# Optimization experiments

Hardware: AMD Instinct MI355X
Metric: run time of the kernel (lower is better)

The kernel has to match this reference:

```python
import jax, jax.numpy as jnp
import numpy as np
import math

B, S, N, F = 512, 72, 5, 10
H, C = 4, 32          # GAT heads, per-head dim
D = H * C             # 128 d_model
L, FF = 3, 256        # transformer layers, ffn dim
K, NS = 6, 5          # horizons, stations
EPS = 1e-5


def layer_norm(x, g, b):
    m = x.mean(-1, keepdims=True)
    v = ((x - m) ** 2).mean(-1, keepdims=True)
    return (x - m) / jnp.sqrt(v + EPS) * g + b


def setup_inputs() -> dict:
    key = jax.random.key(0)
    ks = jax.random.split(key, 16)
    # all 20 directed non-self edges of the 5-node graph
    src, dst = np.nonzero(1 - np.eye(N, dtype=np.int32))
    edge_index = jnp.asarray(np.stack([src, dst]).astype(np.int32))
    w = lambda k, shp: (jax.random.normal(k, shp, jnp.float32) * 0.05)
    return {
        "x": jax.random.normal(ks[0], (B, S, N, F), jnp.float32),
        "edge_index": edge_index,
        "gat_w": w(ks[1], (F, D)),
        "gat_att_src": w(ks[2], (H, C)),
        "gat_att_dst": w(ks[3], (H, C)),
        "gat_bias": jnp.zeros((D,), jnp.float32),
        "gat_ln_g": jnp.ones((D,), jnp.float32),
        "gat_ln_b": jnp.zeros((D,), jnp.float32),
        "qkv_w": w(ks[4], (L, 3 * D, D)),
        "qkv_b": jnp.zeros((L, 3 * D), jnp.float32),
        "out_w": w(ks[5], (L, D, D)),
        "out_b": jnp.zeros((L, D), jnp.float32),
        "ln1_g": jnp.ones((L, D), jnp.float32),
        "ln1_b": jnp.zeros((L, D), jnp.float32),
        "ff1_w": w(ks[6], (L, FF, D)),
        "ff1_b": jnp.zeros((L, FF), jnp.float32),
        "ff2_w": w(ks[7], (L, D, FF)),
        "ff2_b": jnp.zeros((L, D), jnp.float32),
        "ln2_g": jnp.ones((L, D), jnp.float32),
        "ln2_b": jnp.zeros((L, D), jnp.float32),
        "h1_w": w(ks[8], (K, D // 2, D)),
        "h1_b": jnp.zeros((K, D // 2), jnp.float32),
        "h2_w": w(ks[9], (K, NS, D // 2)),
        "h2_b": jnp.zeros((K, NS), jnp.float32),
    }


def reference(x, edge_index, gat_w, gat_att_src, gat_att_dst, gat_bias,
              gat_ln_g, gat_ln_b, qkv_w, qkv_b, out_w, out_b,
              ln1_g, ln1_b, ff1_w, ff1_b, ff2_w, ff2_b, ln2_g, ln2_b,
              h1_w, h1_b, h2_w, h2_b):
    G = B * S                                  # number of independent graphs
    xf = x.reshape(G, N, F)
    # GATConv: per-node projection then edge-softmax attention per destination
    h = jnp.einsum('gnf,fhc->gnhc', xf, gat_w.reshape(F, H, C))   # [G,N,H,C]
    a_src = jnp.einsum('gnhc,hc->gnh', h, gat_att_src)
    a_dst = jnp.einsum('gnhc,hc->gnh', h, gat_att_dst)
    # add self loops (GATConv default; input has no self loops)
    loops = jnp.arange(N, dtype=edge_index.dtype)
    src = jnp.concatenate([edge_index[0], loops])   # [E2]
    dst = jnp.concatenate([edge_index[1], loops])
    e = jax.nn.leaky_relu(a_src[:, src] + a_dst[:, dst], 0.2)     # [G,E2,H]
    et = e.transpose(1, 0, 2)                                     # [E2,G,H]
    m = jax.ops.segment_max(et, dst, num_segments=N)              # [N,G,H]
    ex = jnp.exp(et - m[dst])
    denom = jax.ops.segment_sum(ex, dst, num_segments=N)          # [N,G,H]
    alpha = ex / denom[dst]                                       # [E2,G,H]
    msg = alpha[..., None] * h[:, src].transpose(1, 0, 2, 3)      # [E2,G,H,C]
    agg = jax.ops.segment_sum(msg, dst, num_segments=N)           # [N,G,H,C]
    gat_out = agg.transpose(1, 0, 2, 3).reshape(G, N, D) + gat_bias
    gat_out = layer_norm(gat_out, gat_ln_g, gat_ln_b)

    # mean-pool over nodes -> temporal sequence [B,S,D]
    t = gat_out.reshape(B, S, N, D).mean(axis=2)

    # sinusoidal positional encoding
    pos = jnp.arange(S, dtype=jnp.float32)[:, None]
    div = jnp.exp(jnp.arange(0, D, 2, dtype=jnp.float32) * (-math.log(10000.0) / D))
    pe = jnp.zeros((S, D), jnp.float32)
    pe = pe.at[:, 0::2].set(jnp.sin(pos * div)).at[:, 1::2].set(jnp.cos(pos * div))
    t = t + pe

    scale = 1.0 / math.sqrt(D // H)
    for l in range(L):
        qkv = t @ qkv_w[l].T + qkv_b[l]                 # [B,S,3D]
        q, k, v = jnp.split(qkv, 3, axis=-1)
        q = q.reshape(B, S, H, D // H)
        k = k.reshape(B, S, H, D // H)
        v = v.reshape(B, S, H, D // H)
        scores = jnp.einsum('bqhd,bkhd->bhqk', q, k) * scale
        att = jax.nn.softmax(scores, axis=-1)
        o = jnp.einsum('bhqk,bkhd->bqhd', att, v).reshape(B, S, D)
        o = o @ out_w[l].T + out_b[l]
        t = layer_norm(t + o, ln1_g[l], ln1_b[l])       # post-norm
        f = jax.nn.relu(t @ ff1_w[l].T + ff1_b[l]) @ ff2_w[l].T + ff2_b[l]
        t = layer_norm(t + f, ln2_g[l], ln2_b[l])

    x_last = t[:, -1, :]                                # [B,D]
    h1 = jax.nn.relu(jnp.einsum('bd,kod->kbo', x_last, h1_w) + h1_b[:, None, :])
    out = jnp.einsum('kbo,kpo->kbp', h1, h2_w) + h2_b[:, None, :]
    return out  # [K=6 horizons, B, NS=5]
```

## Files before the change

kernel.cpp:

```cpp
#include <hip/hip_runtime.h>
#include <math.h>

constexpr int B_ = 512, S_ = 72, N_ = 5, F_ = 10;
constexpr int H_ = 4, C_ = 32, D_ = 128;
constexpr int L_ = 3, FF_ = 256;
constexpr int K_ = 6, NS_ = 5;
constexpr int G_ = B_ * S_;
constexpr float EPS_ = 1e-5f;
constexpr int SP_ = 80;
constexpr int KP_ = 96;

constexpr int WQKV_ = 0;
constexpr int WOUT_ = 147456;
constexpr int WFF1_ = 196608;
constexpr int WFF2_ = 294912;
constexpr int WTOT_ = 393216;

typedef short bf16x8 __attribute__((ext_vector_type(8)));
typedef float f32x4 __attribute__((ext_vector_type(4)));

__device__ __forceinline__ short f2bf(float f) {
    unsigned int u = __float_as_uint(f);
    u += 0x7FFFu + ((u >> 16) & 1u);
    return (short)(u >> 16);
}

__global__ __launch_bounds__(128) void pe_kernel(float* __restrict__ pe)
{
    const int s = blockIdx.x;
    const int d = threadIdx.x;
    const float expo = -(float)(d & ~1) * (9.210340371976184f / 128.f);
    const float ang = (float)s * expf(expo);
    pe[s * D_ + d] = (d & 1) ? cosf(ang) : sinf(ang);
}

__global__ __launch_bounds__(128) void gatc_kernel(
    const float* __restrict__ gat_w, const float* __restrict__ att_src,
    const float* __restrict__ att_dst, float* __restrict__ gatc)
{
    const int t = threadIdx.x;
    if (t < 40) {
        const int f = t >> 2, h = t & 3;
        float s = 0.f;
#pragma unroll
        for (int c = 0; c < 32; ++c)
            s = fmaf(gat_w[f * D_ + h * 32 + c], att_src[h * 32 + c], s);
        gatc[t] = s;
    } else if (t < 80) {
        const int f = (t - 40) >> 2, h = (t - 40) & 3;
        float s = 0.f;
#pragma unroll
        for (int c = 0; c < 32; ++c)
            s = fmaf(gat_w[f * D_ + h * 32 + c], att_dst[h * 32 + c], s);
        gatc[t] = s;
    }
}

__global__ __launch_bounds__(256) void wcvt_kernel(
    const float* __restrict__ qw, const float* __restrict__ ow,
    const float* __restrict__ f1, const float* __restrict__ f2,
    short* __restrict__ wb)
{
    const int i4 = (blockIdx.x * 256 + threadIdx.x) * 4;
    const float* src; int off;
    if (i4 < WOUT_)      { src = qw; off = i4; }
    else if (i4 < WFF1_) { src = ow; off = i4 - WOUT_; }
    else if (i4 < WFF2_) { src = f1; off = i4 - WFF1_; }
    else                 { src = f2; off = i4 - WFF2_; }
    const float4 v = *reinterpret_cast<const float4*>(&src[off]);
    short4 h;
    h.x = f2bf(v.x); h.y = f2bf(v.y); h.z = f2bf(v.z); h.w = f2bf(v.w);
    *reinterpret_cast<short4*>(&wb[i4]) = h;
}

__global__ __launch_bounds__(128) void gat_kernel(
    const float* __restrict__ x,
    const float* __restrict__ gat_w,
    const float* __restrict__ gatc,
    const float* __restrict__ gat_bias,
    const float* __restrict__ ln_g,
    const float* __restrict__ ln_b,
    const float* __restrict__ pe,
    float* __restrict__ t_out,
    short* __restrict__ tb_out)
{
    const int g = blockIdx.x;
    const int d = threadIdx.x;
    const int s = g % S_;
    const int head = d >> 5;

    __shared__ float xs[N_][F_];
    __shared__ float red[N_][2][2];

    if (d < N_ * F_) xs[d / F_][d % F_] = x[(size_t)g * N_ * F_ + d];
    __syncthreads();

    float wcol[F_], wsrcv[F_], wdstv[F_];
#pragma unroll
    for (int f = 0; f < F_; ++f) {
        wcol[f]  = gat_w[f * D_ + d];
        wsrcv[f] = gatc[f * 4 + head];
        wdstv[f] = gatc[40 + f * 4 + head];
    }

    float hn[N_], a_s[N_], a_d[N_];
#pragma unroll
    for (int n = 0; n < N_; ++n) {
        float acc = 0.f, ss = 0.f, dd = 0.f;
#pragma unroll
        for (int f = 0; f < F_; ++f) {
            const float xv = xs[n][f];
            acc = fmaf(xv, wcol[f], acc);
            ss  = fmaf(xv, wsrcv[f], ss);
            dd  = fmaf(xv, wdstv[f], dd);
        }
        hn[n] = acc; a_s[n] = ss; a_d[n] = dd;
    }

    float y[N_];
#pragma unroll
    for (int n = 0; n < N_; ++n) {
        const float ad = a_d[n];
        float e[N_];
        float mx = -1e30f;
#pragma unroll
        for (int m = 0; m < N_; ++m) {
            float v = a_s[m] + ad;
            v = v > 0.f ? v : 0.2f * v;
            e[m] = v;
            mx = fmaxf(mx, v);
        }
        float den = 0.f;
#pragma unroll
        for (int m = 0; m < N_; ++m) { e[m] = __expf(e[m] - mx); den += e[m]; }
        const float inv = 1.f / den;
        float agg = 0.f;
#pragma unroll
        for (int m = 0; m < N_; ++m) agg = fmaf(e[m] * inv, hn[m], agg);
        y[n] = agg + gat_bias[d];
    }

    const int wave = d >> 6;
#pragma unroll
    for (int n = 0; n < N_; ++n) {
        float sm = y[n];
        float sq = y[n] * y[n];
#pragma unroll
        for (int off = 32; off >= 1; off >>= 1) {
            sm += __shfl_xor(sm, off);
            sq += __shfl_xor(sq, off);
        }
        if ((d & 63) == 0) { red[n][wave][0] = sm; red[n][wave][1] = sq; }
    }
    __syncthreads();

    const float gg = ln_g[d];
    const float bb = ln_b[d];
    float tacc = 0.f;
#pragma unroll
    for (int n = 0; n < N_; ++n) {
        const float sm = red[n][0][0] + red[n][1][0];
        const float sq = red[n][0][1] + red[n][1][1];
        const float mean = sm * (1.f / D_);
        const float var = sq * (1.f / D_) - mean * mean;
        const float rstd = rsqrtf(var + EPS_);
        tacc += (y[n] - mean) * rstd * gg + bb;
    }
    tacc *= (1.f / N_);

    const float val = tacc + pe[s * D_ + d];
    t_out[(size_t)g * D_ + d] = val;
    tb_out[(size_t)g * D_ + d] = f2bf(val);
}

__global__ __launch_bounds__(256) void linear_mfma_kernel(
    const short* __restrict__ A, const short* __restrict__ W,
    const float* __restrict__ bias, short* __restrict__ out,
    int K, int Cout, int relu)
{
    __shared__ short As[64 * 64];
    __shared__ short Ws[64 * 64];

    const int tid = threadIdx.x;
    const int lane = tid & 63;
    const int wid = tid >> 6;
    const int wr = wid >> 1;
    const int wc = wid & 1;
    const int r0 = blockIdx.x * 64;
    const int c0 = blockIdx.y * 64;

    const int st_row = tid >> 3;
    const int st_slot = tid & 7;

    f32x4 acc[2][2] = {};

    for (int kk = 0; kk < K; kk += 64) {
        if (kk) __syncthreads();
#pragma unroll
        for (int it = 0; it < 2; ++it) {
            const int row = st_row + it * 32;
            const int gk = kk + st_slot * 8;
            const int pslot = st_slot ^ (row & 7);
            *reinterpret_cast<bf16x8*>(&As[row * 64 + pslot * 8]) =
                *reinterpret_cast<const bf16x8*>(&A[(size_t)(r0 + row) * K + gk]);
            *reinterpret_cast<bf16x8*>(&Ws[row * 64 + pslot * 8]) =
                *reinterpret_cast<const bf16x8*>(&W[(size_t)(c0 + row) * K + gk]);
        }
        __syncthreads();

#pragma unroll
        for (int j = 0; j < 2; ++j) {
            bf16x8 aF[2], bF[2];
#pragma unroll
            for (int m = 0; m < 2; ++m) {
                const int row = wr * 32 + m * 16 + (lane & 15);
                const int slot = j * 4 + (lane >> 4);
                const int pslot = slot ^ (row & 7);
                aF[m] = *reinterpret_cast<const bf16x8*>(&As[row * 64 + pslot * 8]);
            }
#pragma unroll
            for (int n = 0; n < 2; ++n) {
                const int col = wc * 32 + n * 16 + (lane & 15);
                const int slot = j * 4 + (lane >> 4);
                const int pslot = slot ^ (col & 7);
                bF[n] = *reinterpret_cast<const bf16x8*>(&Ws[col * 64 + pslot * 8]);
            }
#pragma unroll
            for (int m = 0; m < 2; ++m)
#pragma unroll
                for (int n = 0; n < 2; ++n)
                    acc[m][n] = __builtin_amdgcn_mfma_f32_16x16x32_bf16(
                        aF[m], bF[n], acc[m][n], 0, 0, 0);
        }
    }

#pragma unroll
    for (int m = 0; m < 2; ++m) {
#pragma unroll
        for (int n = 0; n < 2; ++n) {
            const int col = c0 + wc * 32 + n * 16 + (lane & 15);
            const float bv = bias[col];
#pragma unroll
            for (int j = 0; j < 4; ++j) {
                const int row = r0 + wr * 32 + m * 16 + (lane >> 4) * 4 + j;
                float v = acc[m][n][j] + bv;
                if (relu) v = fmaxf(v, 0.f);
                out[(size_t)row * Cout + col] = f2bf(v);
            }
        }
    }
}

__global__ __launch_bounds__(256) void linear_ln_kernel(
    const short* __restrict__ A, const short* __restrict__ W,
    const float* __restrict__ bias, float* __restrict__ t,
    short* __restrict__ tb,
    const float* __restrict__ lng, const float* __restrict__ lnb,
    int K)
{
    __shared__ short As[64 * 64];
    __shared__ short Ws2[128 * 64];
    __shared__ float red[64][2][2];

    const int tid = threadIdx.x;
    const int lane = tid & 63;
    const int wid = tid >> 6;
    const int wr = wid >> 1;
    const int wc = wid & 1;
    const int c16 = lane & 15;
    const int grp = lane >> 4;
    const int r0 = blockIdx.x * 64;

    const int st_row = tid >> 3;
    const int st_slot = tid & 7;

    f32x4 acc[2][4] = {};

    for (int kk = 0; kk < K; kk += 64) {
        if (kk) __syncthreads();
#pragma unroll
        for (int it = 0; it < 2; ++it) {
            const int row = st_row + it * 32;
            const int gk = kk + st_slot * 8;
            const int pslot = st_slot ^ (row & 7);
            *reinterpret_cast<bf16x8*>(&As[row * 64 + pslot * 8]) =
                *reinterpret_cast<const bf16x8*>(&A[(size_t)(r0 + row) * K + gk]);
        }
#pragma unroll
        for (int it = 0; it < 4; ++it) {
            const int row = st_row + it * 32;
            const int gk = kk + st_slot * 8;
            const int pslot = st_slot ^ (row & 7);
            *reinterpret_cast<bf16x8*>(&Ws2[row * 64 + pslot * 8]) =
                *reinterpret_cast<const bf16x8*>(&W[(size_t)row * K + gk]);
        }
        __syncthreads();

#pragma unroll
        for (int j = 0; j < 2; ++j) {
            bf16x8 aF[2], bF[4];
#pragma unroll
            for (int m = 0; m < 2; ++m) {
                const int row = wr * 32 + m * 16 + c16;
                const int slot = j * 4 + grp;
                const int pslot = slot ^ (row & 7);
                aF[m] = *reinterpret_cast<const bf16x8*>(&As[row * 64 + pslot * 8]);
            }
#pragma unroll
            for (int n = 0; n < 4; ++n) {
                const int col = wc * 64 + n * 16 + c16;
                const int slot = j * 4 + grp;
                const int pslot = slot ^ (col & 7);
                bF[n] = *reinterpret_cast<const bf16x8*>(&Ws2[col * 64 + pslot * 8]);
            }
#pragma unroll
            for (int m = 0; m < 2; ++m)
#pragma unroll
                for (int n = 0; n < 4; ++n)
                    acc[m][n] = __builtin_amdgcn_mfma_f32_16x16x32_bf16(
                        aF[m], bF[n], acc[m][n], 0, 0, 0);
        }
    }

#pragma unroll
    for (int m = 0; m < 2; ++m) {
#pragma unroll
        for (int j = 0; j < 4; ++j) {
            const int row = wr * 32 + m * 16 + 4 * grp + j;
            float sm = 0.f, sq = 0.f;
#pragma unroll
            for (int n = 0; n < 4; ++n) {
                const int col = wc * 64 + n * 16 + c16;
                float v = acc[m][n][j] + bias[col]
                        + t[(size_t)(r0 + row) * D_ + col];
                acc[m][n][j] = v;
                sm += v;
                sq += v * v;
            }
#pragma unroll
            for (int off = 8; off >= 1; off >>= 1) {
                sm += __shfl_xor(sm, off);
                sq += __shfl_xor(sq, off);
            }
            if (c16 == 0) { red[row][wc][0] = sm; red[row][wc][1] = sq; }
        }
    }
    __syncthreads();

#pragma unroll
    for (int m = 0; m < 2; ++m) {
#pragma unroll
        for (int j = 0; j < 4; ++j) {
            const int row = wr * 32 + m * 16 + 4 * grp + j;
            const float sm = red[row][0][0] + red[row][1][0];
            const float sq = red[row][0][1] + red[row][1][1];
            const float mean = sm * (1.f / D_);
            const float var = sq * (1.f / D_) - mean * mean;
            const float rstd = rsqrtf(var + EPS_);
#pragma unroll
            for (int n = 0; n < 4; ++n) {
                const int col = wc * 64 + n * 16 + c16;
                const float o = (acc[m][n][j] - mean) * rstd * lng[col] + lnb[col];
                t[(size_t)(r0 + row) * D_ + col] = o;
                tb[(size_t)(r0 + row) * D_ + col] = f2bf(o);
            }
        }
    }
}

__global__ __launch_bounds__(256) void attn_mfma_kernel(
    const short* __restrict__ qkv, short* __restrict__ o)
{
    const int bh = blockIdx.x;
    const int b = bh >> 2;
    const int h = bh & 3;

    __shared__ short Qs[SP_ * 32];
    __shared__ short Ks[SP_ * 32];
    __shared__ short VT[32 * KP_];
    __shared__ short Pb[SP_ * KP_];

    const int tid = threadIdx.x;
    const int lane = tid & 63;
    const int wid = tid >> 6;
    const int g = lane >> 4;
    const int c16 = lane & 15;

    const float scale = 0.17677669529663687f;

    for (int idx = tid; idx < S_ * 4; idx += 256) {
        const int i = idx >> 2;
        const int c8 = (idx & 3) * 8;
        const size_t base = ((size_t)(b * S_ + i)) * 384 + h * 32 + c8;
        const bf16x8 q = *reinterpret_cast<const bf16x8*>(&qkv[base]);
        const bf16x8 k = *reinterpret_cast<const bf16x8*>(&qkv[base + 128]);
        const bf16x8 v = *reinterpret_cast<const bf16x8*>(&qkv[base + 256]);
        *reinterpret_cast<bf16x8*>(&Qs[i * 32 + c8]) = q;
        *reinterpret_cast<bf16x8*>(&Ks[i * 32 + c8]) = k;
#pragma unroll
        for (int j = 0; j < 8; ++j) VT[(c8 + j) * KP_ + i] = v[j];
    }
    for (int idx = tid; idx < 8 * 32; idx += 256) {
        Qs[S_ * 32 + idx] = 0;
        Ks[S_ * 32 + idx] = 0;
    }
    for (int idx = tid; idx < 32 * 24; idx += 256) {
        VT[(idx / 24) * KP_ + 72 + idx % 24] = 0;
    }
    for (int idx = tid; idx < SP_ * 24; idx += 256) {
        Pb[(idx / 24) * KP_ + 72 + idx % 24] = 0;
    }
    __syncthreads();

    float invr[2][4];
#pragma unroll
    for (int mi = 0; mi < 2; ++mi) {
        const int m = wid + 4 * mi;
        if (m <= 4) {
            const int rowb = m * 16;
            const bf16x8 aF = *reinterpret_cast<const bf16x8*>(
                &Qs[(rowb + c16) * 32 + 8 * g]);
            f32x4 sc[5];
#pragma unroll
            for (int n = 0; n < 5; ++n) {
                const bf16x8 bF = *reinterpret_cast<const bf16x8*>(
                    &Ks[(n * 16 + c16) * 32 + 8 * g]);
                f32x4 z = {};
                sc[n] = __builtin_amdgcn_mfma_f32_16x16x32_bf16(aF, bF, z, 0, 0, 0);
                sc[n] = sc[n] * scale;
            }
#pragma unroll
            for (int j = 0; j < 4; ++j) {
                float mx = -1e30f;
#pragma unroll
                for (int n = 0; n < 5; ++n) {
                    const int col = n * 16 + c16;
                    if (col < S_) mx = fmaxf(mx, sc[n][j]);
                }
                mx = fmaxf(mx, __shfl_xor(mx, 1));
                mx = fmaxf(mx, __shfl_xor(mx, 2));
                mx = fmaxf(mx, __shfl_xor(mx, 4));
                mx = fmaxf(mx, __shfl_xor(mx, 8));
                float den = 0.f;
                float p[5];
#pragma unroll
                for (int n = 0; n < 5; ++n) {
                    const int col = n * 16 + c16;
                    p[n] = (col < S_) ? __expf(sc[n][j] - mx) : 0.f;
                    den += p[n];
                }
                den += __shfl_xor(den, 1);
                den += __shfl_xor(den, 2);
                den += __shfl_xor(den, 4);
                den += __shfl_xor(den, 8);
                invr[mi][j] = 1.f / den;
                const int row = rowb + 4 * g + j;
#pragma unroll
                for (int n = 0; n < 5; ++n)
                    Pb[row * KP_ + n * 16 + c16] = f2bf(p[n]);
            }
        }
    }
    __syncthreads();

#pragma unroll
    for (int mi = 0; mi < 2; ++mi) {
        const int m = wid + 4 * mi;
        if (m <= 4) {
            const int rowb = m * 16;
            f32x4 accO[2] = {};
#pragma unroll
            for (int kk = 0; kk < 3; ++kk) {
                const bf16x8 aF = *reinterpret_cast<const bf16x8*>(
                    &Pb[(rowb + c16) * KP_ + kk * 32 + 8 * g]);
#pragma unroll
                for (int n2 = 0; n2 < 2; ++n2) {
                    const bf16x8 bF = *reinterpret_cast<const bf16x8*>(
                        &VT[(n2 * 16 + c16) * KP_ + kk * 32 + 8 * g]);
                    accO[n2] = __builtin_amdgcn_mfma_f32_16x16x32_bf16(
                        aF, bF, accO[n2], 0, 0, 0);
                }
            }
#pragma unroll
            for (int j = 0; j < 4; ++j) {
                const int row = rowb + 4 * g + j;
                if (row < S_) {
                    const float inv = invr[mi][j];
#pragma unroll
                    for (int n2 = 0; n2 < 2; ++n2) {
                        o[((size_t)(b * S_ + row)) * D_ + h * 32 + n2 * 16 + c16]
                            = f2bf(accO[n2][j] * inv);
                    }
                }
            }
        }
    }
}

__global__ __launch_bounds__(64) void head_kernel(
    const float* __restrict__ t, const float* __restrict__ h1_w,
    const float* __restrict__ h1_b, const float* __restrict__ h2_w,
    const float* __restrict__ h2_b, float* __restrict__ out)
{
    const int kb = blockIdx.x;
    const int k = kb / B_;
    const int b = kb - k * B_;
    const int o = threadIdx.x;

    const float* xr = &t[((size_t)(b * S_ + S_ - 1)) * D_];
    const float* wr = &h1_w[((size_t)k * 64 + o) * D_];
    float acc = h1_b[k * 64 + o];
#pragma unroll 8
    for (int d = 0; d < D_; ++d) acc = fmaf(xr[d], wr[d], acc);
    const float h1v = fmaxf(acc, 0.f);

#pragma unroll
    for (int p = 0; p < NS_; ++p) {
        float partial = h1v * h2_w[((size_t)k * NS_ + p) * 64 + o];
#pragma unroll
        for (int off = 32; off >= 1; off >>= 1) partial += __shfl_xor(partial, off);
        if (o == 0) out[((size_t)k * B_ + b) * NS_ + p] = partial + h2_b[k * NS_ + p];
    }
}

extern "C" void kernel_launch(void* const* d_in, const int* in_sizes, int n_in,
                              void* d_out, int out_size, void* d_ws, size_t ws_size,
                              hipStream_t stream) {
    const float* x        = (const float*)d_in[0];
    const float* gat_w    = (const float*)d_in[2];
    const float* att_src  = (const float*)d_in[3];
    const float* att_dst  = (const float*)d_in[4];
    const float* gat_bias = (const float*)d_in[5];
    const float* gat_ln_g = (const float*)d_in[6];
    const float* gat_ln_b = (const float*)d_in[7];
    const float* qkv_w    = (const float*)d_in[8];
    const float* qkv_b    = (const float*)d_in[9];
    const float* out_w    = (const float*)d_in[10];
    const float* out_b    = (const float*)d_in[11];
    const float* ln1_g    = (const float*)d_in[12];
    const float* ln1_b    = (const float*)d_in[13];
    const float* ff1_w    = (const float*)d_in[14];
    const float* ff1_b    = (const float*)d_in[15];
    const float* ff2_w    = (const float*)d_in[16];
    const float* ff2_b    = (const float*)d_in[17];
    const float* ln2_g    = (const float*)d_in[18];
    const float* ln2_b    = (const float*)d_in[19];
    const float* h1_w     = (const float*)d_in[20];
    const float* h1_b     = (const float*)d_in[21];
    const float* h2_w     = (const float*)d_in[22];
    const float* h2_b     = (const float*)d_in[23];
    float* out = (float*)d_out;

    float* base = (float*)d_ws;
    float* t     = base;               base += (size_t)G_ * D_;
    short* qkvb  = (short*)base;       base += (size_t)G_ * 192;
    short* fbufb = (short*)base;       base += (size_t)G_ * 128;
    short* tb    = (short*)base;       base += (size_t)G_ * 64;
    float* pe    = base;               base += (size_t)S_ * D_;
    float* gatc  = base;               base += 128;
    short* wb    = (short*)base;

    pe_kernel<<<S_, 128, 0, stream>>>(pe);
    gatc_kernel<<<1, 128, 0, stream>>>(gat_w, att_src, att_dst, gatc);
    wcvt_kernel<<<WTOT_ / 1024, 256, 0, stream>>>(qkv_w, out_w, ff1_w, ff2_w, wb);
    gat_kernel<<<G_, 128, 0, stream>>>(x, gat_w, gatc,
                                       gat_bias, gat_ln_g, gat_ln_b, pe, t, tb);

    const short* wq = wb + WQKV_;
    const short* wo = wb + WOUT_;
    const short* w1 = wb + WFF1_;
    const short* w2 = wb + WFF2_;

    for (int l = 0; l < L_; ++l) {
        linear_mfma_kernel<<<dim3(G_ / 64, 384 / 64), 256, 0, stream>>>(
            tb, wq + (size_t)l * 384 * D_, qkv_b + (size_t)l * 384, qkvb,
            D_, 384, 0);
        attn_mfma_kernel<<<B_ * H_, 256, 0, stream>>>(qkvb, fbufb);
        linear_ln_kernel<<<G_ / 64, 256, 0, stream>>>(
            fbufb, wo + (size_t)l * D_ * D_, out_b + (size_t)l * D_, t, tb,
            ln1_g + l * D_, ln1_b + l * D_, D_);
        linear_mfma_kernel<<<dim3(G_ / 64, FF_ / 64), 256, 0, stream>>>(
            tb, w1 + (size_t)l * FF_ * D_, ff1_b + (size_t)l * FF_, fbufb,
            D_, FF_, 1);
        linear_ln_kernel<<<G_ / 64, 256, 0, stream>>>(
            fbufb, w2 + (size_t)l * D_ * FF_, ff2_b + (size_t)l * D_, t, tb,
            ln2_g + l * D_, ln2_b + l * D_, FF_);
    }

    head_kernel<<<K_ * B_, 64, 0, stream>>>(t, h1_w, h1_b, h2_w, h2_b, out);
}
```

Before: 418.6 us.

## Share GAT attention coefficients via LDS and enlarge linear kernel row tile

In the GAT kernel, the per-node source/destination attention scores and the edge softmax are now computed once per node and head by a few threads and shared through LDS. Previously all 128 threads recomputed them redundantly. Separately, the generic MFMA linear kernel now processes 128 rows per block instead of 64, with each wave doing a 4x2 MFMA tile. This reuses each loaded weight tile across twice as many rows and halves the grid, at the cost of more registers and LDS per block and two extra barriers in the GAT kernel.

```diff
diff --git a/kernel.cpp b/kernel.cpp
--- a/kernel.cpp
+++ b/kernel.cpp
@@ -90,42 +90,47 @@
     const int head = d >> 5;
 
     __shared__ float xs[N_][F_];
+    __shared__ float ash[N_][H_];
+    __shared__ float adh[N_][H_];
+    __shared__ float al[N_][N_][H_];
     __shared__ float red[N_][2][2];
 
     if (d < N_ * F_) xs[d / F_][d % F_] = x[(size_t)g * N_ * F_ + d];
     __syncthreads();
 
-    float wcol[F_], wsrcv[F_], wdstv[F_];
-#pragma unroll
-    for (int f = 0; f < F_; ++f) {
-        wcol[f]  = gat_w[f * D_ + d];
-        wsrcv[f] = gatc[f * 4 + head];
-        wdstv[f] = gatc[40 + f * 4 + head];
-    }
-
-    float hn[N_], a_s[N_], a_d[N_];
+    if (d < 40) {
+        const int isdst = (d >= 20);
+        const int idx = isdst ? d - 20 : d;
+        const int n = idx >> 2, h = idx & 3;
+        const float* wtab = gatc + (isdst ? 40 : 0);
+        float acc = 0.f;
+#pragma unroll
+        for (int f = 0; f < F_; ++f)
+            acc = fmaf(xs[n][f], wtab[f * 4 + h], acc);
+        if (isdst) adh[n][h] = acc; else ash[n][h] = acc;
+    }
+
+    float wcol[F_];
+#pragma unroll
+    for (int f = 0; f < F_; ++f) wcol[f] = gat_w[f * D_ + d];
+    float hn[N_];
 #pragma unroll
     for (int n = 0; n < N_; ++n) {
-        float acc = 0.f, ss = 0.f, dd = 0.f;
-#pragma unroll
-        for (int f = 0; f < F_; ++f) {
-            const float xv = xs[n][f];
-            acc = fmaf(xv, wcol[f], acc);
-            ss  = fmaf(xv, wsrcv[f], ss);
-            dd  = fmaf(xv, wdstv[f], dd);
-        }
-        hn[n] = acc; a_s[n] = ss; a_d[n] = dd;
-    }
-
-    float y[N_];
-#pragma unroll
-    for (int n = 0; n < N_; ++n) {
-        const float ad = a_d[n];
+        float acc = 0.f;
+#pragma unroll
+        for (int f = 0; f < F_; ++f) acc = fmaf(xs[n][f], wcol[f], acc);
+        hn[n] = acc;
+    }
+    __syncthreads();
+
+    if (d < 20) {
+        const int n = d >> 2, h = d & 3;
+        const float ad = adh[n][h];
         float e[N_];
         float mx = -1e30f;
 #pragma unroll
         for (int m = 0; m < N_; ++m) {
-            float v = a_s[m] + ad;
+            float v = ash[m][h] + ad;
             v = v > 0.f ? v : 0.2f * v;
             e[m] = v;
             mx = fmaxf(mx, v);
@@ -134,10 +139,19 @@
 #pragma unroll
         for (int m = 0; m < N_; ++m) { e[m] = __expf(e[m] - mx); den += e[m]; }
         const float inv = 1.f / den;
+#pragma unroll
+        for (int m = 0; m < N_; ++m) al[n][m][h] = e[m] * inv;
+    }
+    __syncthreads();
+
+    const float bv = gat_bias[d];
+    float y[N_];
+#pragma unroll
+    for (int n = 0; n < N_; ++n) {
         float agg = 0.f;
 #pragma unroll
-        for (int m = 0; m < N_; ++m) agg = fmaf(e[m] * inv, hn[m], agg);
-        y[n] = agg + gat_bias[d];
+        for (int m = 0; m < N_; ++m) agg = fmaf(al[n][m][head], hn[m], agg);
+        y[n] = agg + bv;
     }
 
     const int wave = d >> 6;
@@ -178,7 +192,7 @@
     const float* __restrict__ bias, short* __restrict__ out,
     int K, int Cout, int relu)
 {
-    __shared__ short As[64 * 64];
+    __shared__ short As[128 * 64];
     __shared__ short Ws[64 * 64];
 
     const int tid = threadIdx.x;
@@ -186,23 +200,29 @@
     const int wid = tid >> 6;
     const int wr = wid >> 1;
     const int wc = wid & 1;
-    const int r0 = blockIdx.x * 64;
+    const int r0 = blockIdx.x * 128;
     const int c0 = blockIdx.y * 64;
 
     const int st_row = tid >> 3;
     const int st_slot = tid & 7;
 
-    f32x4 acc[2][2] = {};
+    f32x4 acc[4][2] = {};
 
     for (int kk = 0; kk < K; kk += 64) {
         if (kk) __syncthreads();
 #pragma unroll
-        for (int it = 0; it < 2; ++it) {
+        for (int it = 0; it < 4; ++it) {
             const int row = st_row + it * 32;
             const int gk = kk + st_slot * 8;
             const int pslot = st_slot ^ (row & 7);
             *reinterpret_cast<bf16x8*>(&As[row * 64 + pslot * 8]) =
                 *reinterpret_cast<const bf16x8*>(&A[(size_t)(r0 + row) * K + gk]);
+        }
+#pragma unroll
+        for (int it = 0; it < 2; ++it) {
+            const int row = st_row + it * 32;
+            const int gk = kk + st_slot * 8;
+            const int pslot = st_slot ^ (row & 7);
             *reinterpret_cast<bf16x8*>(&Ws[row * 64 + pslot * 8]) =
                 *reinterpret_cast<const bf16x8*>(&W[(size_t)(c0 + row) * K + gk]);
         }
@@ -210,10 +230,10 @@
 
 #pragma unroll
         for (int j = 0; j < 2; ++j) {
-            bf16x8 aF[2], bF[2];
-#pragma unroll
-            for (int m = 0; m < 2; ++m) {
-                const int row = wr * 32 + m * 16 + (lane & 15);
+            bf16x8 aF[4], bF[2];
+#pragma unroll
+            for (int m = 0; m < 4; ++m) {
+                const int row = wr * 64 + m * 16 + (lane & 15);
                 const int slot = j * 4 + (lane >> 4);
                 const int pslot = slot ^ (row & 7);
                 aF[m] = *reinterpret_cast<const bf16x8*>(&As[row * 64 + pslot * 8]);
@@ -226,7 +246,7 @@
                 bF[n] = *reinterpret_cast<const bf16x8*>(&Ws[col * 64 + pslot * 8]);
             }
 #pragma unroll
-            for (int m = 0; m < 2; ++m)
+            for (int m = 0; m < 4; ++m)
 #pragma unroll
                 for (int n = 0; n < 2; ++n)
                     acc[m][n] = __builtin_amdgcn_mfma_f32_16x16x32_bf16(
@@ -235,14 +255,14 @@
     }
 
 #pragma unroll
-    for (int m = 0; m < 2; ++m) {
+    for (int m = 0; m < 4; ++m) {
 #pragma unroll
         for (int n = 0; n < 2; ++n) {
             const int col = c0 + wc * 32 + n * 16 + (lane & 15);
             const float bv = bias[col];
 #pragma unroll
             for (int j = 0; j < 4; ++j) {
-                const int row = r0 + wr * 32 + m * 16 + (lane >> 4) * 4 + j;
+                const int row = r0 + wr * 64 + m * 16 + (lane >> 4) * 4 + j;
                 float v = acc[m][n][j] + bv;
                 if (relu) v = fmaxf(v, 0.f);
                 out[(size_t)row * Cout + col] = f2bf(v);
@@ -572,14 +592,14 @@
     const short* w2 = wb + WFF2_;
 
     for (int l = 0; l < L_; ++l) {
-        linear_mfma_kernel<<<dim3(G_ / 64, 384 / 64), 256, 0, stream>>>(
+        linear_mfma_kernel<<<dim3(G_ / 128, 384 / 64), 256, 0, stream>>>(
             tb, wq + (size_t)l * 384 * D_, qkv_b + (size_t)l * 384, qkvb,
             D_, 384, 0);
         attn_mfma_kernel<<<B_ * H_, 256, 0, stream>>>(qkvb, fbufb);
         linear_ln_kernel<<<G_ / 64, 256, 0, stream>>>(
             fbufb, wo + (size_t)l * D_ * D_, out_b + (size_t)l * D_, t, tb,
             ln1_g + l * D_, ln1_b + l * D_, D_);
-        linear_mfma_kernel<<<dim3(G_ / 64, FF_ / 64), 256, 0, stream>>>(
+        linear_mfma_kernel<<<dim3(G_ / 128, FF_ / 64), 256, 0, stream>>>(
             tb, w1 + (size_t)l * FF_ * D_, ff1_b + (size_t)l * FF_, fbufb,
             D_, FF_, 1);
         linear_ln_kernel<<<G_ / 64, 256, 0, stream>>>(
```

Measured after the change: 393.8 us. 1.06x faster.
